# Performance work log

Measured on AMD Instinct MI355X. Metric: run time of the kernel, lower is better.

Reference implementation:

```python
import jax, jax.numpy as jnp
import numpy as np

N_NODES = 50000
N_EDGES = 800000
IN_DIM = 128
OUT_DIM = 16
N_HEADS = 4
NEG_SLOPE = 0.01  # jax.nn.leaky_relu default, matches original


def setup_inputs() -> dict:
    key = jax.random.key(0)
    k = jax.random.split(key, 8)
    nodes = jax.random.normal(k[0], (N_NODES, IN_DIM), dtype=jnp.float32)
    edges = jax.random.uniform(k[1], (N_NODES, 1), dtype=jnp.float32)  # node-indexed edge attr (edges[senders] in source)
    senders = jax.random.randint(k[2], (N_EDGES,), 0, N_NODES, dtype=jnp.int32)
    receivers = jax.random.randint(k[3], (N_EDGES,), 0, N_NODES, dtype=jnp.int32)
    W = jax.random.normal(k[4], (N_HEADS * OUT_DIM, IN_DIM), dtype=jnp.float32) / np.sqrt(IN_DIM)
    b = jnp.zeros((N_HEADS * OUT_DIM,), dtype=jnp.float32)
    attn_W = jax.random.normal(k[5], (N_HEADS, 2 * OUT_DIM + 1), dtype=jnp.float32) / np.sqrt(2 * OUT_DIM + 1)
    attn_b = jnp.zeros((N_HEADS,), dtype=jnp.float32)
    return dict(nodes=nodes, edges=edges, senders=senders, receivers=receivers,
                W=W, b=b, attn_W=attn_W, attn_b=attn_b)


def _segment_softmax(logits, seg, num_segments):
    # logits: [E, H, 1]; softmax over edges sharing the same receiver
    m = jax.ops.segment_max(logits, seg, num_segments=num_segments)
    e = jnp.exp(logits - m[seg])
    s = jax.ops.segment_sum(e, seg, num_segments=num_segments)
    return e / s[seg]


def reference(nodes, edges, senders, receivers, W, b, attn_W, attn_b):
    n = nodes.shape[0]
    h = (nodes @ W.T + b).reshape(n, N_HEADS, OUT_DIM)       # [N, H, D]
    sent = h[senders]                                        # [E, H, D]
    recv = h[receivers]                                      # [E, H, D]
    sent_e = jnp.tile(edges[senders], (1, N_HEADS))[..., None]  # [E, H, 1]
    feat = jnp.concatenate([sent, recv, sent_e], axis=-1)    # [E, H, 2D+1]
    logits = (jnp.einsum('ehd,hd->eh', feat, attn_W) + attn_b)[..., None]  # [E, H, 1]
    logits = jax.nn.leaky_relu(logits, NEG_SLOPE)
    logits = logits * jnp.sum(sent_e)                        # scalar scaling as in source
    att = _segment_softmax(logits, receivers, n)             # [E, H, 1]
    msg = sent * att                                         # [E, H, D]
    out = jax.ops.segment_sum(msg, receivers, num_segments=n)  # [N, H, D]
    out = jax.nn.leaky_relu(out, NEG_SLOPE)                  # last=False branch
    return out.reshape(n, N_HEADS * OUT_DIM)
```

## Files before the change

### kernel.cpp

```cpp
#include <hip/hip_runtime.h>
#include <math.h>

#define N_NODES 50000
#define N_EDGES 800000
#define IN_DIM 128
#define OUT_DIM 16
#define N_HEADS 4
#define HID 64
#define AW_COLS 33
#define GN 32
#define GEMM_BLK ((N_NODES + GN - 1) / GN)
#define HE 16
#define HBLK ((N_EDGES + 256 * HE - 1) / (256 * HE))
#define MAXDEG 64

__global__ __launch_bounds__(256) void gemm_hist(
    const float* __restrict__ nodes, const float* __restrict__ W,
    const float* __restrict__ b, const float* __restrict__ attn_W,
    const float* __restrict__ attn_b, const float* __restrict__ edges,
    float* __restrict__ h, double* __restrict__ z_src, double* __restrict__ z_dst,
    const int* __restrict__ senders, const int* __restrict__ receivers,
    int* __restrict__ counts, int* __restrict__ srt_padded,
    double* __restrict__ Ssum) {
    __shared__ float sW[HID * IN_DIM];
    __shared__ float sN[GN * IN_DIM];
    int t = threadIdx.x;

    if (blockIdx.x < HBLK) {
        double* red = (double*)sN;
        int base = blockIdx.x * 256 * HE + t;
        double sp = 0.0;
        #pragma unroll
        for (int j = 0; j < HE; ++j) {
            int e = base + j * 256;
            if (e < N_EDGES) {
                int r = receivers[e];
                int rank = atomicAdd(&counts[r], 1);
                if (rank < MAXDEG)
                    srt_padded[r * MAXDEG + rank] = senders[e];
                sp += (double)edges[senders[e]];
            }
        }
        red[t] = sp;
        __syncthreads();
        for (int off = 128; off > 0; off >>= 1) {
            if (t < off) red[t] += red[t + off];
            __syncthreads();
        }
        if (t == 0) atomicAdd(Ssum, red[0]);
    } else {
        for (int i4 = t; i4 < HID * IN_DIM / 4; i4 += 256) {
            int o = i4 >> 5, kq = i4 & 31;
            float4 v = ((const float4*)W)[i4];
            *(float4*)&sW[o * IN_DIM + (((kq + o) & 31) << 2)] = v;
        }
        int node0 = (blockIdx.x - HBLK) * GN;
        for (int i4 = t; i4 < GN * IN_DIM / 4; i4 += 256) {
            int ln = i4 >> 5;
            int n = node0 + ln;
            float4 v = (n < N_NODES) ? ((const float4*)nodes)[(long long)n * (IN_DIM / 4) + (i4 & 31)]
                                     : make_float4(0.f, 0.f, 0.f, 0.f);
            *(float4*)&sN[i4 << 2] = v;
        }
        __syncthreads();
        int w = t >> 6, l = t & 63;
        int half = l >> 5;
        int o2 = l & 31;
        int nwbase = w * 8 + half * 4;
        double acc0[4], acc1[4];
        double b0 = (double)b[o2], b1 = (double)b[o2 + 32];
        #pragma unroll
        for (int j = 0; j < 4; ++j) { acc0[j] = b0; acc1[j] = b1; }
        const float* wrow0 = &sW[o2 * IN_DIM];
        const float* wrow1 = &sW[(o2 + 32) * IN_DIM];
        const float* nbase = &sN[nwbase * IN_DIM];
        for (int kq = 0; kq < 32; ++kq) {
            int rot = ((kq + o2) & 31) << 2;
            float4 wv0 = *(const float4*)&wrow0[rot];
            float4 wv1 = *(const float4*)&wrow1[rot];
            double w0x = (double)wv0.x, w0y = (double)wv0.y, w0z = (double)wv0.z, w0w = (double)wv0.w;
            double w1x = (double)wv1.x, w1y = (double)wv1.y, w1z = (double)wv1.z, w1w = (double)wv1.w;
            #pragma unroll
            for (int j = 0; j < 4; ++j) {
                float4 nv = *(const float4*)&nbase[j * IN_DIM + (kq << 2)];
                double nx = (double)nv.x, ny = (double)nv.y;
                double nz = (double)nv.z, nw = (double)nv.w;
                acc0[j] += w0x * nx; acc0[j] += w0y * ny;
                acc0[j] += w0z * nz; acc0[j] += w0w * nw;
                acc1[j] += w1x * nx; acc1[j] += w1y * ny;
                acc1[j] += w1z * nz; acc1[j] += w1w * nw;
            }
        }
        int hd0 = o2 >> 4, d = o2 & 15;
        int hd1 = hd0 + 2;
        double aw00 = (double)attn_W[hd0 * AW_COLS + d];
        double aw01 = (double)attn_W[hd0 * AW_COLS + OUT_DIM + d];
        double aw10 = (double)attn_W[hd1 * AW_COLS + d];
        double aw11 = (double)attn_W[hd1 * AW_COLS + OUT_DIM + d];
        double wE0 = (double)attn_W[hd0 * AW_COLS + 2 * OUT_DIM];
        double wE1 = (double)attn_W[hd1 * AW_COLS + 2 * OUT_DIM];
        double bb0 = (double)attn_b[hd0], bb1 = (double)attn_b[hd1];
        #pragma unroll
        for (int j = 0; j < 4; ++j) {
            int n = node0 + nwbase + j;
            if (n >= N_NODES) continue;
            float hf0 = (float)acc0[j];
            float hf1 = (float)acc1[j];
            h[(long long)n * HID + o2] = hf0;
            h[(long long)n * HID + o2 + 32] = hf1;
            double c00 = (double)hf0 * aw00;
            double c01 = (double)hf0 * aw01;
            double c10 = (double)hf1 * aw10;
            double c11 = (double)hf1 * aw11;
            #pragma unroll
            for (int k = 1; k <= 8; k <<= 1) {
                c00 += __shfl_xor(c00, k, 64);
                c01 += __shfl_xor(c01, k, 64);
                c10 += __shfl_xor(c10, k, 64);
                c11 += __shfl_xor(c11, k, 64);
            }
            if (d == 0) {
                double se = (double)edges[n];
                z_src[n * N_HEADS + hd0] = c00 + se * wE0;
                z_dst[n * N_HEADS + hd0] = c01 + bb0;
                z_src[n * N_HEADS + hd1] = c10 + se * wE1;
                z_dst[n * N_HEADS + hd1] = c11 + bb1;
            }
        }
    }
}

__global__ __launch_bounds__(256) void node_fused(
    const float* __restrict__ h, const double* __restrict__ z_src,
    const double* __restrict__ z_dst,
    const int* __restrict__ srt_padded, const int* __restrict__ counts,
    const double* __restrict__ Ssum, float* __restrict__ out) {
    int node = blockIdx.x * 4 + (threadIdx.x >> 6);
    int lane = threadIdx.x & 63;
    if (node >= N_NODES) return;
    int hd = lane >> 4, q = lane & 15;
    int deg = counts[node];
    if (deg > MAXDEG) deg = MAXDEG;
    long long obase = (long long)node * HID + lane;
    if (deg <= 0) { out[obase] = 0.f; return; }
    const int* srow = srt_padded + node * MAXDEG;

    double S = 4.0 * Ssum[0];
    double zdn = z_dst[node * N_HEADS + hd];
    float den = 0.f, acc = 0.f;

    int s[4];
    float y[4], ev[4];
    #pragma unroll
    for (int j = 0; j < 4; ++j) {
        int ei = q + 16 * j;
        y[j] = -INFINITY;
        s[j] = 0;
        if (ei < deg) {
            s[j] = srow[ei];
            double yy = z_src[(long long)s[j] * N_HEADS + hd] + zdn;
            yy = yy > 0.0 ? yy : 0.01 * yy;
            y[j] = (float)yy;
        }
    }
    float mv = fmaxf(fmaxf(y[0], y[1]), fmaxf(y[2], y[3]));
    #pragma unroll
    for (int k = 1; k <= 8; k <<= 1)
        mv = fmaxf(mv, __shfl_xor(mv, k, 64));
    float m_run = mv;
    float dsum = 0.f;
    #pragma unroll
    for (int j = 0; j < 4; ++j) {
        ev[j] = (y[j] == -INFINITY) ? 0.f
              : __expf((float)(S * ((double)y[j] - (double)m_run)));
        dsum += ev[j];
    }
    #pragma unroll
    for (int k = 1; k <= 8; k <<= 1)
        dsum += __shfl_xor(dsum, k, 64);
    den += dsum;
    #pragma unroll
    for (int j = 0; j < 4; ++j) {
        unsigned long long mk = __ballot(ev[j] != 0.f);
        unsigned um = (unsigned)((mk | (mk >> 16) | (mk >> 32) | (mk >> 48)) & 0xFFFFull);
        while (um) {
            int qq = __builtin_ctz(um);
            um &= um - 1;
            int src = (lane & 48) | qq;
            float evv = __shfl(ev[j], src, 64);
            int sj = __shfl(s[j], src, 64);
            if (evv != 0.f)
                acc = fmaf(evv, h[(long long)sj * HID + lane], acc);
        }
    }
    float r = (den > 0.f) ? acc / den : 0.f;
    out[obase] = r > 0.f ? r : 0.01f * r;
}

static inline char* ws_take(char*& p, size_t bytes) {
    char* cur = p;
    p += (bytes + 255) & ~(size_t)255;
    return cur;
}

extern "C" void kernel_launch(void* const* d_in, const int* in_sizes, int n_in,
                              void* d_out, int out_size, void* d_ws, size_t ws_size,
                              hipStream_t stream) {
    const float* nodes     = (const float*)d_in[0];
    const float* edges     = (const float*)d_in[1];
    const int*   senders   = (const int*)d_in[2];
    const int*   receivers = (const int*)d_in[3];
    const float* W         = (const float*)d_in[4];
    const float* b         = (const float*)d_in[5];
    const float* attn_W    = (const float*)d_in[6];
    const float* attn_b    = (const float*)d_in[7];
    float* out = (float*)d_out;

    char* p = (char*)d_ws;
    float*  h          = (float*)ws_take(p, sizeof(float) * N_NODES * HID);
    double* z_src      = (double*)ws_take(p, sizeof(double) * N_NODES * N_HEADS);
    double* z_dst      = (double*)ws_take(p, sizeof(double) * N_NODES * N_HEADS);
    int*    counts     = (int*)ws_take(p, sizeof(int) * N_NODES);
    char*   zpad       = ws_take(p, 256);
    double* Ssum       = (double*)zpad;
    int*    srt_padded = (int*)ws_take(p, sizeof(int) * (size_t)N_NODES * MAXDEG);

    hipMemsetAsync(counts, 0, ((sizeof(int) * N_NODES + 255) & ~(size_t)255) + 256, stream);

    gemm_hist<<<HBLK + GEMM_BLK, 256, 0, stream>>>(
        nodes, W, b, attn_W, attn_b, edges, h, z_src, z_dst,
        senders, receivers, counts, srt_padded, Ssum);
    node_fused<<<(N_NODES + 3) / 4, 256, 0, stream>>>(
        h, z_src, z_dst, srt_padded, counts, Ssum, out);
}
```

Measured before the change: 162.4 us.

## Halve GEMM node tile, add occupancy hint and software-prefetch LDS operands

Reduces the GEMM tile from 32 to 16 nodes per block, so each thread keeps 2 instead of 4 double accumulators, and requests 4 blocks per CU via launch bounds. The k-loop now double-buffers its shared-memory reads by loading the next iteration's W and node float4s before computing the current one. The aim is higher occupancy and hidden LDS latency in the FP64 GEMM. The cost is loading the full W matrix into LDS twice as often across twice as many blocks, and less data reuse per W load.

```diff
diff --git a/kernel.cpp b/kernel.cpp
--- a/kernel.cpp
+++ b/kernel.cpp
@@ -8,13 +8,13 @@
 #define N_HEADS 4
 #define HID 64
 #define AW_COLS 33
-#define GN 32
+#define GN 16
 #define GEMM_BLK ((N_NODES + GN - 1) / GN)
 #define HE 16
 #define HBLK ((N_EDGES + 256 * HE - 1) / (256 * HE))
 #define MAXDEG 64
 
-__global__ __launch_bounds__(256) void gemm_hist(
+__global__ __launch_bounds__(256, 4) void gemm_hist(
     const float* __restrict__ nodes, const float* __restrict__ W,
     const float* __restrict__ b, const float* __restrict__ attn_W,
     const float* __restrict__ attn_b, const float* __restrict__ edges,
@@ -66,30 +66,45 @@
         int w = t >> 6, l = t & 63;
         int half = l >> 5;
         int o2 = l & 31;
-        int nwbase = w * 8 + half * 4;
-        double acc0[4], acc1[4];
+        int nwbase = w * 4 + half * 2;
+        double acc0[2], acc1[2];
         double b0 = (double)b[o2], b1 = (double)b[o2 + 32];
         #pragma unroll
-        for (int j = 0; j < 4; ++j) { acc0[j] = b0; acc1[j] = b1; }
+        for (int j = 0; j < 2; ++j) { acc0[j] = b0; acc1[j] = b1; }
         const float* wrow0 = &sW[o2 * IN_DIM];
         const float* wrow1 = &sW[(o2 + 32) * IN_DIM];
         const float* nbase = &sN[nwbase * IN_DIM];
+        int rot0 = (o2 & 31) << 2;
+        float4 wv0 = *(const float4*)&wrow0[rot0];
+        float4 wv1 = *(const float4*)&wrow1[rot0];
+        float4 nva = *(const float4*)&nbase[0];
+        float4 nvb = *(const float4*)&nbase[IN_DIM];
         for (int kq = 0; kq < 32; ++kq) {
-            int rot = ((kq + o2) & 31) << 2;
-            float4 wv0 = *(const float4*)&wrow0[rot];
-            float4 wv1 = *(const float4*)&wrow1[rot];
+            int kn = (kq + 1) & 31;
+            int rotn = ((kn + o2) & 31) << 2;
+            float4 wv0n = *(const float4*)&wrow0[rotn];
+            float4 wv1n = *(const float4*)&wrow1[rotn];
+            float4 nvan = *(const float4*)&nbase[kn << 2];
+            float4 nvbn = *(const float4*)&nbase[IN_DIM + (kn << 2)];
             double w0x = (double)wv0.x, w0y = (double)wv0.y, w0z = (double)wv0.z, w0w = (double)wv0.w;
             double w1x = (double)wv1.x, w1y = (double)wv1.y, w1z = (double)wv1.z, w1w = (double)wv1.w;
-            #pragma unroll
-            for (int j = 0; j < 4; ++j) {
-                float4 nv = *(const float4*)&nbase[j * IN_DIM + (kq << 2)];
-                double nx = (double)nv.x, ny = (double)nv.y;
-                double nz = (double)nv.z, nw = (double)nv.w;
-                acc0[j] += w0x * nx; acc0[j] += w0y * ny;
-                acc0[j] += w0z * nz; acc0[j] += w0w * nw;
-                acc1[j] += w1x * nx; acc1[j] += w1y * ny;
-                acc1[j] += w1z * nz; acc1[j] += w1w * nw;
-            }
+            {
+                double nx = (double)nva.x, ny = (double)nva.y;
+                double nz = (double)nva.z, nw = (double)nva.w;
+                acc0[0] += w0x * nx; acc0[0] += w0y * ny;
+                acc0[0] += w0z * nz; acc0[0] += w0w * nw;
+                acc1[0] += w1x * nx; acc1[0] += w1y * ny;
+                acc1[0] += w1z * nz; acc1[0] += w1w * nw;
+            }
+            {
+                double nx = (double)nvb.x, ny = (double)nvb.y;
+                double nz = (double)nvb.z, nw = (double)nvb.w;
+                acc0[1] += w0x * nx; acc0[1] += w0y * ny;
+                acc0[1] += w0z * nz; acc0[1] += w0w * nw;
+                acc1[1] += w1x * nx; acc1[1] += w1y * ny;
+                acc1[1] += w1z * nz; acc1[1] += w1w * nw;
+            }
+            wv0 = wv0n; wv1 = wv1n; nva = nvan; nvb = nvbn;
         }
         int hd0 = o2 >> 4, d = o2 & 15;
         int hd1 = hd0 + 2;
@@ -101,7 +116,7 @@
         double wE1 = (double)attn_W[hd1 * AW_COLS + 2 * OUT_DIM];
         double bb0 = (double)attn_b[hd0], bb1 = (double)attn_b[hd1];
         #pragma unroll
-        for (int j = 0; j < 4; ++j) {
+        for (int j = 0; j < 2; ++j) {
             int n = node0 + nwbase + j;
             if (n >= N_NODES) continue;
             float hf0 = (float)acc0[j];
```

New measurement: 161.9 us. No clear change (-0.3%).
